# Kernel tuning notes

Hardware: AMD Instinct MI355X
Metric: run time of the kernel (lower is better)

Reference implementation:

```python
import jax, jax.numpy as jnp
import numpy as np

NUM_EXPERTS = 64
NUM_SELECTED = 2
HASH_BITS = 32


def setup_inputs() -> dict:
    key = jax.random.key(0)
    k1, k2 = jax.random.split(key)
    hidden_states = jax.random.normal(k1, (4, 4096, 2048), dtype=jnp.float32)
    # torch Linear weight [out_features, in_features], init normal(std=0.01), bias zeros
    hash_w = jax.random.normal(k2, (NUM_SELECTED * HASH_BITS, 2048), dtype=jnp.float32) * 0.01
    hash_b = jnp.zeros((NUM_SELECTED * HASH_BITS,), dtype=jnp.float32)
    return {"hidden_states": hidden_states, "hash_w": hash_w, "hash_b": hash_b}


def reference(hidden_states, hash_w, hash_b):
    B, S, H = hidden_states.shape
    T = B * S
    x = hidden_states.reshape(T, H)
    # hash projection: [T, k*32]
    h = x @ hash_w.T + hash_b
    bits = (h > 0).astype(jnp.int32).reshape(T, NUM_SELECTED, HASH_BITS)
    cand = bits.sum(axis=-1) % NUM_EXPERTS  # [T, k] candidate expert per slot

    # Sequential dedup (vectorized over tokens): for each slot i in order, if the
    # candidate collides with an already-chosen expert for that token, advance
    # (e+1) % E until a free expert is found (always exists since k <= E).
    used = jnp.zeros((T, NUM_EXPERTS), dtype=bool)
    offs = jnp.arange(NUM_EXPERTS)
    chosen = []
    for i in range(NUM_SELECTED):
        e = cand[:, i]  # [T]
        pos = (e[:, None] + offs[None, :]) % NUM_EXPERTS  # [T, E] probe sequence
        probed = jnp.take_along_axis(used, pos, axis=1)  # [T, E] used flags along probe
        off = jnp.argmax(~probed, axis=1)  # first free offset (0 if candidate free)
        ne = (e + off) % NUM_EXPERTS
        used = used | jax.nn.one_hot(ne, NUM_EXPERTS, dtype=bool)
        chosen.append(ne)
    expert_indices = jnp.stack(chosen, axis=1).astype(jnp.int32)  # [T, k]
    expert_weights = jnp.full((T, NUM_SELECTED), 1.0 / NUM_SELECTED, dtype=jnp.float32)
    router_logits = jnp.zeros((T, NUM_EXPERTS), dtype=jnp.float32)
    return expert_weights, expert_indices, router_logits
```

## Files before the change

### kernel.cpp

```cpp
#include <hip/hip_runtime.h>


constexpr int H_DIM  = 2048;
constexpr int NJ     = 64;
constexpr int TOK    = 32;
constexpr int KC     = 64;
constexpr int NCHUNK = H_DIM / KC;
constexpr int XF     = TOK * KC;
constexpr int WF     = NJ * KC;
constexpr int BUF    = XF + WF;
constexpr int XSLOTS = XF / 4;

__device__ __forceinline__ int sw_of(int row) {
    return (3 * (row >> 3) + ((row >> 2) & 1)) & 7;
}

__device__ __forceinline__ void stage_chunk(const float* __restrict__ x,
                                            const float* __restrict__ w,
                                            float* smem, int fb,
                                            int tok0, int k0, int tid) {
#pragma unroll
    for (int it = 0; it < 6; ++it) {
        const int slot = it * 256 + tid;
        const float* g;
        if (slot < XSLOTS) {
            const int row = slot >> 4, c4p = slot & 15;
            g = x + (size_t)(tok0 + row) * H_DIM + k0 + ((c4p ^ sw_of(row)) << 2);
        } else {
            const int s2 = slot - XSLOTS;
            const int row = s2 >> 4, c4p = s2 & 15;
            g = w + (size_t)row * H_DIM + k0 + ((c4p ^ sw_of(row)) << 2);
        }
        __builtin_amdgcn_global_load_lds(
            (const __attribute__((address_space(1))) void*)g,
            (__attribute__((address_space(3))) void*)(smem + fb + slot * 4),
            16, 0, 0);
    }
}

__global__ __launch_bounds__(256, 2) void hash_router_kernel(
    const float* __restrict__ x,
    const float* __restrict__ w,
    const float* __restrict__ b,
    float* __restrict__ out,
    int T)
{
    __shared__ float smem[2 * BUF];
    __shared__ unsigned int bitw[TOK][2];

    const int tid = threadIdx.x;
    const int og  = tid & 7;
    const int tg  = (tid >> 3) & 3;
    const int kg  = tid >> 5;
    const int tok0 = blockIdx.x * TOK;

    if (tid < TOK * 2) ((unsigned int*)bitw)[tid] = 0u;

    float acc[8][8];
#pragma unroll
    for (int i = 0; i < 8; ++i)
#pragma unroll
        for (int j = 0; j < 8; ++j) acc[i][j] = 0.f;

    stage_chunk(x, w, smem, 0, tok0, 0, tid);

    for (int ch = 0; ch < NCHUNK; ++ch) {
        __builtin_amdgcn_s_waitcnt(0x0f70);
        __syncthreads();
        if (ch + 1 < NCHUNK)
            stage_chunk(x, w, smem, ((ch + 1) & 1) * BUF, tok0, (ch + 1) * KC, tid);

        const int fb = (ch & 1) * BUF;
#pragma unroll
        for (int c = 0; c < 2; ++c) {
            const int k4 = kg * 2 + c;
            float4 xv[8];
#pragma unroll
            for (int i = 0; i < 8; ++i) {
                const int row = tg * 8 + i;
                xv[i] = *(const float4*)(smem + fb + row * KC + ((k4 ^ sw_of(row)) << 2));
            }
#pragma unroll
            for (int j = 0; j < 8; ++j) {
                const int row = og * 8 + j;
                const float4 wv = *(const float4*)(smem + fb + XF + row * KC + ((k4 ^ sw_of(row)) << 2));
#pragma unroll
                for (int i = 0; i < 8; ++i) {
                    acc[i][j] += xv[i].x * wv.x;
                    acc[i][j] += xv[i].y * wv.y;
                    acc[i][j] += xv[i].z * wv.z;
                    acc[i][j] += xv[i].w * wv.w;
                }
            }
        }
    }

    __syncthreads();
    const int s  = tid & 31;
    const int sw = s & 7;
#define ACC_PACK(f4) make_float4(acc[(f4) >> 1][((f4) & 1) * 4],     \
                                 acc[(f4) >> 1][((f4) & 1) * 4 + 1], \
                                 acc[(f4) >> 1][((f4) & 1) * 4 + 2], \
                                 acc[(f4) >> 1][((f4) & 1) * 4 + 3])
#define ACC_ADD(f4, v) { acc[(f4) >> 1][((f4) & 1) * 4]     += (v).x; \
                         acc[(f4) >> 1][((f4) & 1) * 4 + 1] += (v).y; \
                         acc[(f4) >> 1][((f4) & 1) * 4 + 2] += (v).z; \
                         acc[(f4) >> 1][((f4) & 1) * 4 + 3] += (v).w; }
    if (kg >= 4) {
        float* base = smem + ((kg - 4) * 32 + s) * 64;
#pragma unroll
        for (int f4 = 0; f4 < 16; ++f4) *(float4*)(base + ((f4 ^ sw) << 2)) = ACC_PACK(f4);
    }
    __syncthreads();
    if (kg < 4) {
        const float* base = smem + (kg * 32 + s) * 64;
#pragma unroll
        for (int f4 = 0; f4 < 16; ++f4) { float4 v = *(const float4*)(base + ((f4 ^ sw) << 2)); ACC_ADD(f4, v); }
    }
    __syncthreads();
    if (kg == 2 || kg == 3) {
        float* base = smem + ((kg - 2) * 32 + s) * 64;
#pragma unroll
        for (int f4 = 0; f4 < 16; ++f4) *(float4*)(base + ((f4 ^ sw) << 2)) = ACC_PACK(f4);
    }
    __syncthreads();
    if (kg < 2) {
        const float* base = smem + (kg * 32 + s) * 64;
#pragma unroll
        for (int f4 = 0; f4 < 16; ++f4) { float4 v = *(const float4*)(base + ((f4 ^ sw) << 2)); ACC_ADD(f4, v); }
    }
    __syncthreads();
    if (kg == 1) {
        float* base = smem + s * 64;
#pragma unroll
        for (int f4 = 0; f4 < 16; ++f4) *(float4*)(base + ((f4 ^ sw) << 2)) = ACC_PACK(f4);
    }
    __syncthreads();

    if (kg == 0) {
        const float* base = smem + s * 64;
#pragma unroll
        for (int f4 = 0; f4 < 16; ++f4) { float4 v = *(const float4*)(base + ((f4 ^ sw) << 2)); ACC_ADD(f4, v); }

        float bias[8];
#pragma unroll
        for (int j = 0; j < 8; ++j) bias[j] = b[og * 8 + j];

        const float TH = 5e-5f;
#pragma unroll
        for (int i = 0; i < 8; ++i) {
            unsigned int byte = 0u;
#pragma unroll
            for (int j = 0; j < 8; ++j) {
                const float v = acc[i][j] + bias[j];
                bool pos;
                if (__builtin_expect(fabsf(v) < TH, 0)) {
                    const float* xr = x + (size_t)(tok0 + tg * 8 + i) * H_DIM;
                    const float* wr = w + (size_t)(og * 8 + j) * H_DIM;
                    double sd = (double)bias[j];
                    for (int k = 0; k < H_DIM; ++k)
                        sd += (double)xr[k] * (double)wr[k];
                    pos = (sd > 0.0);
                } else {
                    pos = (v > 0.0f);
                }
                byte |= (pos ? 1u : 0u) << j;
            }
            if (byte) atomicOr(&bitw[tg * 8 + i][og >> 2], byte << ((og & 3) * 8));
        }
    }
    __syncthreads();

    if (tid < TOK) {
        const int t  = tok0 + tid;
        const int c0 = __popc(bitw[tid][0]);
        const int c1 = __popc(bitw[tid][1]);
        const int i1 = c1 + ((c1 == c0) ? 1 : 0);
        float2 wq; wq.x = 0.5f; wq.y = 0.5f;
        *(float2*)(out + 2 * (size_t)t) = wq;
        float2 iq; iq.x = (float)c0; iq.y = (float)i1;
        *(float2*)(out + 2 * (size_t)T + 2 * (size_t)t) = iq;
    }

    float4 z; z.x = 0.f; z.y = 0.f; z.z = 0.f; z.w = 0.f;
    float* lbase = out + 4 * (size_t)T + (size_t)tok0 * NJ;
#pragma unroll
    for (int i = tid; i < TOK * NJ / 4; i += 256)
        *(float4*)(lbase + i * 4) = z;
}

extern "C" void kernel_launch(void* const* d_in, const int* in_sizes, int n_in,
                              void* d_out, int out_size, void* d_ws, size_t ws_size,
                              hipStream_t stream) {
    const float* x = (const float*)d_in[0];
    const float* w = (const float*)d_in[1];
    const float* b = (const float*)d_in[2];
    float* out = (float*)d_out;
    const int T = in_sizes[0] / H_DIM;
    const int grid = T / TOK;
    hash_router_kernel<<<dim3(grid), dim3(256), 0, stream>>>(x, w, b, out, T);
}
```

Baseline: 293.2 us.

## Double block size to 512 threads and split K across twice as many lanes

The block grows from 256 to 512 threads, so each thread now covers one float4 K-slice per chunk instead of two. The partial sums are first combined across the two half-waves with a wave shuffle, then by the existing LDS tree reduction, now indexed by wave. The aim is more threads in flight to hide LDS latency. Launch bounds now request 4 blocks of 512 threads, which can force the 64-entry accumulator array plus operands into a tight register budget and risks spills. The LDS footprint per block may also cap how many blocks actually fit.

```diff
diff --git a/kernel.cpp b/kernel.cpp
--- a/kernel.cpp
+++ b/kernel.cpp
@@ -10,6 +10,8 @@
 constexpr int WF     = NJ * KC;
 constexpr int BUF    = XF + WF;
 constexpr int XSLOTS = XF / 4;
+constexpr int NTHR   = 512;
+constexpr int SLOTS  = BUF / 4;
 
 __device__ __forceinline__ int sw_of(int row) {
     return (3 * (row >> 3) + ((row >> 2) & 1)) & 7;
@@ -20,8 +22,8 @@
                                             float* smem, int fb,
                                             int tok0, int k0, int tid) {
 #pragma unroll
-    for (int it = 0; it < 6; ++it) {
-        const int slot = it * 256 + tid;
+    for (int it = 0; it < SLOTS / NTHR; ++it) {
+        const int slot = it * NTHR + tid;
         const float* g;
         if (slot < XSLOTS) {
             const int row = slot >> 4, c4p = slot & 15;
@@ -38,7 +40,7 @@
     }
 }
 
-__global__ __launch_bounds__(256, 2) void hash_router_kernel(
+__global__ __launch_bounds__(NTHR, 4) void hash_router_kernel(
     const float* __restrict__ x,
     const float* __restrict__ w,
     const float* __restrict__ b,
@@ -71,76 +73,81 @@
             stage_chunk(x, w, smem, ((ch + 1) & 1) * BUF, tok0, (ch + 1) * KC, tid);
 
         const int fb = (ch & 1) * BUF;
-#pragma unroll
-        for (int c = 0; c < 2; ++c) {
-            const int k4 = kg * 2 + c;
-            float4 xv[8];
+        const int k4 = kg;
+        float4 xv[8];
+#pragma unroll
+        for (int i = 0; i < 8; ++i) {
+            const int row = tg * 8 + i;
+            xv[i] = *(const float4*)(smem + fb + row * KC + ((k4 ^ sw_of(row)) << 2));
+        }
+#pragma unroll
+        for (int j = 0; j < 8; ++j) {
+            const int row = og * 8 + j;
+            const float4 wv = *(const float4*)(smem + fb + XF + row * KC + ((k4 ^ sw_of(row)) << 2));
 #pragma unroll
             for (int i = 0; i < 8; ++i) {
-                const int row = tg * 8 + i;
-                xv[i] = *(const float4*)(smem + fb + row * KC + ((k4 ^ sw_of(row)) << 2));
+                acc[i][j] += xv[i].x * wv.x;
+                acc[i][j] += xv[i].y * wv.y;
+                acc[i][j] += xv[i].z * wv.z;
+                acc[i][j] += xv[i].w * wv.w;
             }
-#pragma unroll
-            for (int j = 0; j < 8; ++j) {
-                const int row = og * 8 + j;
-                const float4 wv = *(const float4*)(smem + fb + XF + row * KC + ((k4 ^ sw_of(row)) << 2));
-#pragma unroll
-                for (int i = 0; i < 8; ++i) {
-                    acc[i][j] += xv[i].x * wv.x;
-                    acc[i][j] += xv[i].y * wv.y;
-                    acc[i][j] += xv[i].z * wv.z;
-                    acc[i][j] += xv[i].w * wv.w;
-                }
-            }
-        }
-    }
-
-    __syncthreads();
+        }
+    }
+
+    __syncthreads();
+#pragma unroll
+    for (int i = 0; i < 8; ++i)
+#pragma unroll
+        for (int j = 0; j < 8; ++j)
+            acc[i][j] += __shfl_xor(acc[i][j], 32, 64);
+
+    const int v  = tid >> 6;
+    const bool lo = (tid & 32) == 0;
     const int s  = tid & 31;
     const int sw = s & 7;
 #define ACC_PACK(f4) make_float4(acc[(f4) >> 1][((f4) & 1) * 4],     \
                                  acc[(f4) >> 1][((f4) & 1) * 4 + 1], \
                                  acc[(f4) >> 1][((f4) & 1) * 4 + 2], \
                                  acc[(f4) >> 1][((f4) & 1) * 4 + 3])
-#define ACC_ADD(f4, v) { acc[(f4) >> 1][((f4) & 1) * 4]     += (v).x; \
-                         acc[(f4) >> 1][((f4) & 1) * 4 + 1] += (v).y; \
-                         acc[(f4) >> 1][((f4) & 1) * 4 + 2] += (v).z; \
-                         acc[(f4) >> 1][((f4) & 1) * 4 + 3] += (v).w; }
-    if (kg >= 4) {
-        float* base = smem + ((kg - 4) * 32 + s) * 64;
+#define ACC_ADD(f4, val) { acc[(f4) >> 1][((f4) & 1) * 4]     += (val).x; \
+                           acc[(f4) >> 1][((f4) & 1) * 4 + 1] += (val).y; \
+                           acc[(f4) >> 1][((f4) & 1) * 4 + 2] += (val).z; \
+                           acc[(f4) >> 1][((f4) & 1) * 4 + 3] += (val).w; }
+    if (v >= 4 && lo) {
+        float* base = smem + ((v - 4) * 32 + s) * 64;
 #pragma unroll
         for (int f4 = 0; f4 < 16; ++f4) *(float4*)(base + ((f4 ^ sw) << 2)) = ACC_PACK(f4);
     }
     __syncthreads();
-    if (kg < 4) {
-        const float* base = smem + (kg * 32 + s) * 64;
-#pragma unroll
-        for (int f4 = 0; f4 < 16; ++f4) { float4 v = *(const float4*)(base + ((f4 ^ sw) << 2)); ACC_ADD(f4, v); }
-    }
-    __syncthreads();
-    if (kg == 2 || kg == 3) {
-        float* base = smem + ((kg - 2) * 32 + s) * 64;
+    if (v < 4 && lo) {
+        const float* base = smem + (v * 32 + s) * 64;
+#pragma unroll
+        for (int f4 = 0; f4 < 16; ++f4) { float4 t = *(const float4*)(base + ((f4 ^ sw) << 2)); ACC_ADD(f4, t); }
+    }
+    __syncthreads();
+    if ((v == 2 || v == 3) && lo) {
+        float* base = smem + ((v - 2) * 32 + s) * 64;
 #pragma unroll
         for (int f4 = 0; f4 < 16; ++f4) *(float4*)(base + ((f4 ^ sw) << 2)) = ACC_PACK(f4);
     }
     __syncthreads();
-    if (kg < 2) {
-        const float* base = smem + (kg * 32 + s) * 64;
-#pragma unroll
-        for (int f4 = 0; f4 < 16; ++f4) { float4 v = *(const float4*)(base + ((f4 ^ sw) << 2)); ACC_ADD(f4, v); }
-    }
-    __syncthreads();
-    if (kg == 1) {
+    if (v < 2 && lo) {
+        const float* base = smem + (v * 32 + s) * 64;
+#pragma unroll
+        for (int f4 = 0; f4 < 16; ++f4) { float4 t = *(const float4*)(base + ((f4 ^ sw) << 2)); ACC_ADD(f4, t); }
+    }
+    __syncthreads();
+    if (v == 1 && lo) {
         float* base = smem + s * 64;
 #pragma unroll
         for (int f4 = 0; f4 < 16; ++f4) *(float4*)(base + ((f4 ^ sw) << 2)) = ACC_PACK(f4);
     }
     __syncthreads();
 
-    if (kg == 0) {
+    if (v == 0 && lo) {
         const float* base = smem + s * 64;
 #pragma unroll
-        for (int f4 = 0; f4 < 16; ++f4) { float4 v = *(const float4*)(base + ((f4 ^ sw) << 2)); ACC_ADD(f4, v); }
+        for (int f4 = 0; f4 < 16; ++f4) { float4 t = *(const float4*)(base + ((f4 ^ sw) << 2)); ACC_ADD(f4, t); }
 
         float bias[8];
 #pragma unroll
@@ -152,9 +159,9 @@
             unsigned int byte = 0u;
 #pragma unroll
             for (int j = 0; j < 8; ++j) {
-                const float v = acc[i][j] + bias[j];
+                const float hv = acc[i][j] + bias[j];
                 bool pos;
-                if (__builtin_expect(fabsf(v) < TH, 0)) {
+                if (__builtin_expect(fabsf(hv) < TH, 0)) {
                     const float* xr = x + (size_t)(tok0 + tg * 8 + i) * H_DIM;
                     const float* wr = w + (size_t)(og * 8 + j) * H_DIM;
                     double sd = (double)bias[j];
@@ -162,7 +169,7 @@
                         sd += (double)xr[k] * (double)wr[k];
                     pos = (sd > 0.0);
                 } else {
-                    pos = (v > 0.0f);
+                    pos = (hv > 0.0f);
                 }
                 byte |= (pos ? 1u : 0u) << j;
             }
@@ -185,7 +192,7 @@
     float4 z; z.x = 0.f; z.y = 0.f; z.z = 0.f; z.w = 0.f;
     float* lbase = out + 4 * (size_t)T + (size_t)tok0 * NJ;
 #pragma unroll
-    for (int i = tid; i < TOK * NJ / 4; i += 256)
+    for (int i = tid; i < TOK * NJ / 4; i += NTHR)
         *(float4*)(lbase + i * 4) = z;
 }
 
@@ -198,5 +205,5 @@
     float* out = (float*)d_out;
     const int T = in_sizes[0] / H_DIM;
     const int grid = T / TOK;
-    hash_router_kernel<<<dim3(grid), dim3(256), 0, stream>>>(x, w, b, out, T);
-}
+    hash_router_kernel<<<dim3(grid), dim3(NTHR), 0, stream>>>(x, w, b, out, T);
+}
```

New measurement: 345.8 us. +17.9%, slower.
